# Optimization experiments

Measured on AMD Instinct MI355X. Metric: run time of the kernel, lower is better.

## Reference

```python
import jax, jax.numpy as jnp
import numpy as np

C_CURV = 1.0
EPS = 1e-5            # bound_eps from source
MAX_NORM = (1.0 - 1e-5) / (C_CURV ** 0.5)  # Poincare ball projection radius


def _conv3x3(x, w, b):
    # x: (N,Cin,H,W), w: (Cout,Cin,3,3), padding=1 -> SAME
    y = jax.lax.conv_general_dilated(
        x, w, window_strides=(1, 1), padding=((1, 1), (1, 1)),
        dimension_numbers=('NCHW', 'OIHW', 'NCHW'))
    return y + b[None, :, None, None]


def _maxpool2(x):
    return jax.lax.reduce_window(x, -jnp.inf, jax.lax.max,
                                 (1, 1, 2, 2), (1, 1, 2, 2), 'VALID')


def _hyp_mlr(x, w, b):
    # x: (N,D), w: hyperplane_normals (K,D), b: hyperplane_offsets (K,D)
    c = C_CURV
    sqrt_c = c ** 0.5
    x2 = jnp.sum(x * x, axis=-1, keepdims=True)          # (N,1)
    b2 = jnp.sum(b * b, axis=-1)                          # (K,)
    w_norm = jnp.linalg.norm(w, axis=-1)                  # (K,)
    inner_x_b = x @ (-b.T)                                # (N,K)
    a_num = 1.0 + 2.0 * c * inner_x_b + c * x2            # (N,K)
    b_num = 1.0 - c * b2                                  # (K,)
    denom = 1.0 + 2.0 * c * inner_x_b + (c * c) * (x2 * b2[None, :])
    alpha = a_num / jnp.maximum(denom, EPS)
    beta = b_num[None, :] / denom                         # raw denom, as in source
    mob2 = alpha ** 2 * b2[None, :] + 2.0 * alpha * beta * inner_x_b + beta ** 2 * x2
    sq = jnp.sqrt(mob2)
    normalizer = jnp.where(sq > MAX_NORM, MAX_NORM / jnp.maximum(sq, EPS),
                           jnp.ones_like(mob2))
    mob2 = jnp.where(sq < MAX_NORM, mob2, jnp.full_like(mob2, MAX_NORM ** 2))
    wn = w / jnp.maximum(jnp.linalg.norm(w, axis=-1, keepdims=True), 1e-12)
    hyperplane = alpha * jnp.sum(wn * (-b), axis=-1)[None, :] + beta * (x @ wn.T)
    hyperplane = hyperplane * normalizer
    asinh_in = 2.0 * sqrt_c * hyperplane / jnp.maximum(1.0 - c * mob2, EPS)
    scaler = 2.0 / jnp.maximum(1.0 - c * b2, EPS)         # (K,)
    return (1.0 / sqrt_c) * (scaler * w_norm)[None, :] * jnp.arcsinh(asinh_in)


def setup_inputs() -> dict:
    key = jax.random.key(0)
    ks = jax.random.split(key, 8)
    N, D, K = 4096, 32, 10
    x = jax.random.normal(ks[0], (N, 1, 28, 28), dtype=jnp.float32)
    conv1_w = jax.random.normal(ks[1], (32, 1, 3, 3), dtype=jnp.float32) * 0.1
    conv1_b = jnp.zeros((32,), dtype=jnp.float32)
    conv2_w = jax.random.normal(ks[2], (64, 32, 3, 3), dtype=jnp.float32) * 0.05
    conv2_b = jnp.zeros((64,), dtype=jnp.float32)
    fc_w = jax.random.normal(ks[3], (D, 7 * 7 * 64), dtype=jnp.float32) * 0.02
    fc_b = jnp.zeros((D,), dtype=jnp.float32)
    hyp_w = jax.random.normal(ks[4], (K, D), dtype=jnp.float32) * 0.05
    hyp_b = jnp.zeros((K, D), dtype=jnp.float32)
    return dict(x=x, conv1_w=conv1_w, conv1_b=conv1_b, conv2_w=conv2_w,
                conv2_b=conv2_b, fc_w=fc_w, fc_b=fc_b, hyp_w=hyp_w, hyp_b=hyp_b)


def reference(x, conv1_w, conv1_b, conv2_w, conv2_b, fc_w, fc_b, hyp_w, hyp_b):
    h = _maxpool2(jax.nn.relu(_conv3x3(x, conv1_w, conv1_b)))   # (N,32,14,14)
    h = _maxpool2(jax.nn.relu(_conv3x3(h, conv2_w, conv2_b)))   # (N,64,7,7)
    h = h.reshape(h.shape[0], -1)                                # (N,3136)
    h = h @ fc_w.T + fc_b                                        # (N,32)
    return _hyp_mlr(h, hyp_w, hyp_b)                             # (N,10)
```

## Files before the change

kernel.cpp:

```cpp
#include <hip/hip_runtime.h>
#include <math.h>

#define EPSV 1e-5f

typedef _Float16 f16x8 __attribute__((ext_vector_type(8)));
typedef _Float16 f16x4 __attribute__((ext_vector_type(4)));
typedef float f32x4 __attribute__((ext_vector_type(4)));

__global__ __launch_bounds__(256) void prep_weights(
    const float* __restrict__ w1, const float* __restrict__ b1,
    const float* __restrict__ w2, const float* __restrict__ fw,
    _Float16* __restrict__ w2t_hi, _Float16* __restrict__ w2t_lo,
    _Float16* __restrict__ fw_hi,  _Float16* __restrict__ fw_lo,
    _Float16* __restrict__ w1p_hi, _Float16* __restrict__ w1p_lo)
{
    int idx = blockIdx.x * 256 + threadIdx.x;
    if (idx < 18432) {
        int off = idx >> 11;
        int rem = idx & 2047;
        int oc = rem >> 5, ic = rem & 31;
        float v = w2[(oc * 32 + ic) * 9 + off];
        _Float16 hx = (_Float16)v;
        w2t_hi[idx] = hx;
        w2t_lo[idx] = (_Float16)(v - (float)hx);
    } else if (idx < 18432 + 100352) {
        int j = idx - 18432;
        float v = fw[j];
        _Float16 hx = (_Float16)v;
        fw_hi[j] = hx;
        fw_lo[j] = (_Float16)(v - (float)hx);
    } else if (idx < 18432 + 100352 + 1024) {
        int j = idx - (18432 + 100352);
        int oc = j >> 5, k = j & 31;
        float v = (k < 9) ? w1[oc * 9 + k] : ((k == 9) ? b1[oc] : 0.f);
        _Float16 hx = (_Float16)v;
        w1p_hi[j] = hx;
        w1p_lo[j] = (_Float16)(v - (float)hx);
    }
}

__global__ __launch_bounds__(256, 4) void conv_fused(
    const float* __restrict__ x,
    const _Float16* __restrict__ w1p_hi,
    const _Float16* __restrict__ w1p_lo,
    const _Float16* __restrict__ w2t_hi,
    const _Float16* __restrict__ w2t_lo,
    const float* __restrict__ b2,
    _Float16* __restrict__ feat_hi,
    _Float16* __restrict__ feat_lo)
{
    __shared__ float4 smem4[2017];
    unsigned* in_pad  = (unsigned*)smem4;
    _Float16* Bbuf_hi = (_Float16*)((char*)smem4 + 3600);
    _Float16* Bbuf_lo = (_Float16*)((char*)smem4 + 17936);
    _Float16* Fhi     = (_Float16*)smem4;
    _Float16* Flo     = Fhi + 3136;

    const int tid  = threadIdx.x;
    const int lane = tid & 63;
    const int wave = tid >> 6;
    const int kg   = lane >> 4;
    const int cl   = lane & 15;
    const int clr  = (cl < 14) ? cl : 13;
    const int n    = blockIdx.x;

    for (int i = tid; i < 116; i += 256) {
        int yy, xx;
        if (i < 30)       { yy = 0;          xx = i; }
        else if (i < 60)  { yy = 29;         xx = i - 30; }
        else if (i < 88)  { yy = i - 60 + 1; xx = 0; }
        else              { yy = i - 88 + 1; xx = 29; }
        in_pad[yy * 30 + xx] = 0u;
    }
    const float* xin = x + (size_t)n * 784;
    for (int i = tid; i < 784; i += 256) {
        int yy = i / 28, xx = i - yy * 28;
        float v = xin[i];
        _Float16 hx = (_Float16)v;
        _Float16 lx = (_Float16)(v - (float)hx);
        unsigned hb = *(const unsigned short*)&hx;
        unsigned lb = *(const unsigned short*)&lx;
        in_pad[(yy + 1) * 30 + (xx + 1)] = hb | (lb << 16);
    }
    if (tid < 112) {
        int icg = tid / 28, j = tid - icg * 28;
        int row = j >> 1, col = (j & 1) ? 15 : 0;
        int c = (icg * 224 + row * 16 + col) * 8;
        *(f32x4*)(Bbuf_hi + c) = (f32x4){0.f, 0.f, 0.f, 0.f};
        *(f32x4*)(Bbuf_lo + c) = (f32x4){0.f, 0.f, 0.f, 0.f};
    }
    __syncthreads();

    {
        f16x8 a1h[2], a1l[2];
        #pragma unroll
        for (int m = 0; m < 2; ++m) {
            a1h[m] = *(const f16x8*)(w1p_hi + (m * 16 + cl) * 32 + kg * 8);
            a1l[m] = *(const f16x8*)(w1p_lo + (m * 16 + cl) * 32 + kg * 8);
        }
        const int o0 = (kg == 0) ? 0  : ((kg == 1) ? 62 : 0);
        const int o1 = (kg == 0) ? 1  : 0;
        const int o2 = (kg == 0) ? 2  : 0;
        const int o3 = (kg == 0) ? 30 : 0;
        const int o4 = (kg == 0) ? 31 : 0;
        const int o5 = (kg == 0) ? 32 : 0;
        const int o6 = (kg == 0) ? 60 : 0;
        const int o7 = (kg == 0) ? 61 : 0;

        const bool wr = ((cl & 1) == 0) && (cl < 14);

        #pragma unroll 1
        for (int u = 0; u < 7; ++u) {
            const int unit = wave * 7 + u;
            const int rp = unit >> 1, hx = unit & 1;
            const int xcol = hx * 14 + cl;
            f16x8 bh[2], bl[2];
            #pragma unroll
            for (int r2 = 0; r2 < 2; ++r2) {
                const int base = (2 * rp + r2) * 30 + xcol;
                unsigned v0 = in_pad[base + o0], v1 = in_pad[base + o1];
                unsigned v2 = in_pad[base + o2], v3 = in_pad[base + o3];
                unsigned v4 = in_pad[base + o4], v5 = in_pad[base + o5];
                unsigned v6 = in_pad[base + o6], v7 = in_pad[base + o7];
                unsigned h01 = (v0 & 0xFFFFu) | (v1 << 16);
                unsigned h23 = (v2 & 0xFFFFu) | (v3 << 16);
                unsigned h45 = (v4 & 0xFFFFu) | (v5 << 16);
                unsigned h67 = (v6 & 0xFFFFu) | (v7 << 16);
                unsigned l01 = (v0 >> 16) | (v1 & 0xFFFF0000u);
                unsigned l23 = (v2 >> 16) | (v3 & 0xFFFF0000u);
                unsigned l45 = (v4 >> 16) | (v5 & 0xFFFF0000u);
                unsigned l67 = (v6 >> 16) | (v7 & 0xFFFF0000u);
                if (kg == 1) {
                    h01 = (h01 & 0xFFFFu) | 0x3C000000u;
                    l01 = (l01 & 0xFFFFu);
                    h23 = h45 = h67 = 0u; l23 = l45 = l67 = 0u;
                } else if (kg >= 2) {
                    h01 = h23 = h45 = h67 = 0u;
                    l01 = l23 = l45 = l67 = 0u;
                }
                union { unsigned uu[4]; f16x8 v; } uh, ul;
                uh.uu[0] = h01; uh.uu[1] = h23; uh.uu[2] = h45; uh.uu[3] = h67;
                ul.uu[0] = l01; ul.uu[1] = l23; ul.uu[2] = l45; ul.uu[3] = l67;
                bh[r2] = uh.v; bl[r2] = ul.v;
            }
            #pragma unroll
            for (int m = 0; m < 2; ++m) {
                f32x4 a0 = (f32x4){0.f, 0.f, 0.f, 0.f};
                f32x4 a1 = (f32x4){0.f, 0.f, 0.f, 0.f};
                a0 = __builtin_amdgcn_mfma_f32_16x16x32_f16(a1h[m], bh[0], a0, 0, 0, 0);
                a0 = __builtin_amdgcn_mfma_f32_16x16x32_f16(a1l[m], bh[0], a0, 0, 0, 0);
                a0 = __builtin_amdgcn_mfma_f32_16x16x32_f16(a1h[m], bl[0], a0, 0, 0, 0);
                a1 = __builtin_amdgcn_mfma_f32_16x16x32_f16(a1h[m], bh[1], a1, 0, 0, 0);
                a1 = __builtin_amdgcn_mfma_f32_16x16x32_f16(a1l[m], bh[1], a1, 0, 0, 0);
                a1 = __builtin_amdgcn_mfma_f32_16x16x32_f16(a1h[m], bl[1], a1, 0, 0, 0);
                float pv[4];
                #pragma unroll
                for (int r = 0; r < 4; ++r) {
                    float vp = fmaxf(a0[r], a1[r]);
                    float hp = fmaxf(vp, __shfl_xor(vp, 1));
                    pv[r] = fmaxf(hp, 0.f);
                }
                union { unsigned short s[4]; f16x4 v; } ph, pl;
                #pragma unroll
                for (int r = 0; r < 4; ++r) {
                    _Float16 mh = (_Float16)pv[r];
                    _Float16 ml = (_Float16)(pv[r] - (float)mh);
                    ph.s[r] = *(const unsigned short*)&mh;
                    pl.s[r] = *(const unsigned short*)&ml;
                }
                if (wr) {
                    const int px2 = hx * 7 + (cl >> 1);
                    const int cell = ((m * 2 + (kg >> 1)) * 224 +
                                      rp * 16 + (px2 + 1)) * 8 + (kg & 1) * 4;
                    *(f16x4*)(Bbuf_hi + cell) = ph.v;
                    *(f16x4*)(Bbuf_lo + cell) = pl.v;
                }
            }
        }
    }
    __syncthreads();

    const int ocb = wave * 16;
    float bias[4];
    #pragma unroll
    for (int r = 0; r < 4; ++r) bias[r] = b2[ocb + kg * 4 + r];

    f32x4 acc[14];
    #pragma unroll
    for (int r = 0; r < 14; ++r) acc[r] = (f32x4){0.f, 0.f, 0.f, 0.f};

    {
        const size_t arow = (size_t)(ocb + cl) * 32 + kg * 8;
        f16x8 a_hi = *(const f16x8*)(w2t_hi + arow);
        f16x8 a_lo = *(const f16x8*)(w2t_lo + arow);

        #pragma unroll 1
        for (int off = 0; off < 9; ++off) {
            f16x8 na_hi = a_hi, na_lo = a_lo;
            if (off < 8) {
                na_hi = *(const f16x8*)(w2t_hi + arow + (size_t)(off + 1) * 2048);
                na_lo = *(const f16x8*)(w2t_lo + arow + (size_t)(off + 1) * 2048);
            }
            const int ky = off / 3, kx = off - ky * 3;
            const int cbase = (kg * 224 + clr + kx) * 8;
            #pragma unroll
            for (int py = 0; py < 14; ++py) {
                const int g = ky + py;
                if (g >= 1 && g <= 14) {
                    const int addr = cbase + (g - 1) * 128;
                    f16x8 b_hi = *(const f16x8*)(Bbuf_hi + addr);
                    f16x8 b_lo = *(const f16x8*)(Bbuf_lo + addr);
                    acc[py] = __builtin_amdgcn_mfma_f32_16x16x32_f16(a_hi, b_hi, acc[py], 0, 0, 0);
                    acc[py] = __builtin_amdgcn_mfma_f32_16x16x32_f16(a_lo, b_hi, acc[py], 0, 0, 0);
                    acc[py] = __builtin_amdgcn_mfma_f32_16x16x32_f16(a_hi, b_lo, acc[py], 0, 0, 0);
                }
            }
            a_hi = na_hi; a_lo = na_lo;
        }
    }
    __syncthreads();

    {
        const bool wlane = ((cl & 1) == 0) && (cl < 14);
        const int px2 = cl >> 1;
        #pragma unroll
        for (int p = 0; p < 7; ++p) {
            f32x4 r0 = acc[2 * p], r1 = acc[2 * p + 1];
            #pragma unroll
            for (int r = 0; r < 4; ++r) {
                float v0 = fmaxf(r0[r], __shfl_xor(r0[r], 1));
                float v1 = fmaxf(r1[r], __shfl_xor(r1[r], 1));
                float m = fmaxf(fmaxf(v0, v1) + bias[r], 0.f);
                _Float16 mh = (_Float16)m;
                _Float16 ml = (_Float16)(m - (float)mh);
                if (wlane) {
                    int o = (ocb + kg * 4 + r) * 49 + p * 7 + px2;
                    Fhi[o] = mh; Flo[o] = ml;
                }
            }
        }
    }
    __syncthreads();

    unsigned* gh = (unsigned*)(feat_hi + (size_t)n * 3136);
    unsigned* gl = (unsigned*)(feat_lo + (size_t)n * 3136);
    const unsigned* sh = (const unsigned*)Fhi;
    const unsigned* sl = (const unsigned*)Flo;
    for (int i = tid; i < 1568; i += 256) { gh[i] = sh[i]; gl[i] = sl[i]; }
}

__global__ __launch_bounds__(512) void fc_mlr(
    const _Float16* __restrict__ feat_hi, const _Float16* __restrict__ feat_lo,
    const _Float16* __restrict__ fw_hi,   const _Float16* __restrict__ fw_lo,
    const float* __restrict__ fb,
    const float* __restrict__ hw,
    const float* __restrict__ hb,
    float* __restrict__ out)
{
    __shared__ float part[8][64][9];
    __shared__ float Ht[16][33];

    const int tid  = threadIdx.x;
    const int lane = tid & 63;
    const int wave = tid >> 6;
    const int kg = lane >> 4, cl = lane & 15;
    const int m0 = blockIdx.x * 16;

    const int start = (wave < 2) ? wave * 13 : 26 + (wave - 2) * 12;
    const int nstep = (wave < 2) ? 13 : 12;
    const size_t koff = (size_t)start * 32 + kg * 8;

    const _Float16* ah  = feat_hi + (size_t)(m0 + cl) * 3136 + koff;
    const _Float16* al  = feat_lo + (size_t)(m0 + cl) * 3136 + koff;
    const _Float16* b0h = fw_hi + (size_t)cl * 3136 + koff;
    const _Float16* b0l = fw_lo + (size_t)cl * 3136 + koff;
    const _Float16* b1h = fw_hi + (size_t)(16 + cl) * 3136 + koff;
    const _Float16* b1l = fw_lo + (size_t)(16 + cl) * 3136 + koff;

    f32x4 acc0 = {0.f, 0.f, 0.f, 0.f}, acc1 = {0.f, 0.f, 0.f, 0.f};
    for (int s = 0; s < nstep; ++s) {
        int k0 = s * 32;
        f16x8 vah = *(const f16x8*)(ah + k0);
        f16x8 val_ = *(const f16x8*)(al + k0);
        f16x8 v0h = *(const f16x8*)(b0h + k0);
        f16x8 v0l = *(const f16x8*)(b0l + k0);
        f16x8 v1h = *(const f16x8*)(b1h + k0);
        f16x8 v1l = *(const f16x8*)(b1l + k0);
        acc0 = __builtin_amdgcn_mfma_f32_16x16x32_f16(vah, v0h, acc0, 0, 0, 0);
        acc0 = __builtin_amdgcn_mfma_f32_16x16x32_f16(val_, v0h, acc0, 0, 0, 0);
        acc0 = __builtin_amdgcn_mfma_f32_16x16x32_f16(vah, v0l, acc0, 0, 0, 0);
        acc1 = __builtin_amdgcn_mfma_f32_16x16x32_f16(vah, v1h, acc1, 0, 0, 0);
        acc1 = __builtin_amdgcn_mfma_f32_16x16x32_f16(val_, v1h, acc1, 0, 0, 0);
        acc1 = __builtin_amdgcn_mfma_f32_16x16x32_f16(vah, v1l, acc1, 0, 0, 0);
    }
    #pragma unroll
    for (int r = 0; r < 4; ++r) {
        part[wave][lane][r]     = acc0[r];
        part[wave][lane][4 + r] = acc1[r];
    }
    __syncthreads();

    {
        int col = tid & 31, row = tid >> 5;
        int l  = ((row >> 2) << 4) + (col & 15);
        int rr = ((col >= 16) ? 4 : 0) + (row & 3);
        float s = 0.f;
        #pragma unroll
        for (int w = 0; w < 8; ++w) s += part[w][l][rr];
        Ht[row][col] = s + fb[col];
    }
    __syncthreads();

    if (tid < 160) {
        int im = tid / 10, k = tid - im * 10;
        const float* xr = &Ht[im][0];
        const float* wr = hw + k * 32;
        const float* br = hb + k * 32;
        float x2 = 0.f, b2s = 0.f, ww = 0.f, xb = 0.f, xw = 0.f, wb = 0.f;
        #pragma unroll
        for (int i = 0; i < 32; ++i) {
            float xi = xr[i], wi = wr[i], bi = br[i];
            x2 += xi * xi;  b2s += bi * bi;  ww += wi * wi;
            xb += xi * bi;  xw += xi * wi;   wb += wi * bi;
        }
        float w_norm = sqrtf(ww);
        float wnc = fmaxf(w_norm, 1e-12f);
        float inner = -xb;
        float a_num = 1.f + 2.f * inner + x2;
        float b_num = 1.f - b2s;
        float den = 1.f + 2.f * inner + x2 * b2s;
        float alpha = a_num / fmaxf(den, EPSV);
        float beta = b_num / den;
        float mob2 = alpha * alpha * b2s + 2.f * alpha * beta * inner + beta * beta * x2;
        float sq = sqrtf(mob2);
        const float MAXN = (float)(1.0 - 1e-5);
        const float MAXN2 = (float)((1.0 - 1e-5) * (1.0 - 1e-5));
        float normalizer = (sq > MAXN) ? (MAXN / fmaxf(sq, EPSV)) : 1.f;
        float mob2c = (sq < MAXN) ? mob2 : MAXN2;
        float hyper = (alpha * (-wb) + beta * xw) / wnc;
        hyper *= normalizer;
        float asin_in = 2.f * hyper / fmaxf(1.f - mob2c, EPSV);
        float scaler = 2.f / fmaxf(1.f - b2s, EPSV);
        out[(size_t)m0 * 10 + tid] = scaler * w_norm * asinhf(asin_in);
    }
}

extern "C" void kernel_launch(void* const* d_in, const int* in_sizes, int n_in,
                              void* d_out, int out_size, void* d_ws, size_t ws_size,
                              hipStream_t stream) {
    const float* x   = (const float*)d_in[0];
    const float* w1  = (const float*)d_in[1];
    const float* b1  = (const float*)d_in[2];
    const float* w2  = (const float*)d_in[3];
    const float* b2  = (const float*)d_in[4];
    const float* fw  = (const float*)d_in[5];
    const float* fb  = (const float*)d_in[6];
    const float* hw  = (const float*)d_in[7];
    const float* hb  = (const float*)d_in[8];
    float* out = (float*)d_out;

    const int N = 4096;
    char* ws = (char*)d_ws;
    _Float16* feat_hi = (_Float16*)ws;
    _Float16* feat_lo = (_Float16*)(ws + 25690112);
    _Float16* w2t_hi  = (_Float16*)(ws + 51380224);
    _Float16* w2t_lo  = (_Float16*)(ws + 51417088);
    _Float16* fw_hi   = (_Float16*)(ws + 51453952);
    _Float16* fw_lo   = (_Float16*)(ws + 51654656);
    _Float16* w1p_hi  = (_Float16*)(ws + 51855360);
    _Float16* w1p_lo  = (_Float16*)(ws + 51857408);

    prep_weights<<<(18432 + 100352 + 1024 + 255) / 256, 256, 0, stream>>>(
        w1, b1, w2, fw, w2t_hi, w2t_lo, fw_hi, fw_lo, w1p_hi, w1p_lo);
    conv_fused<<<N, 256, 0, stream>>>(x, w1p_hi, w1p_lo, w2t_hi, w2t_lo, b2,
                                      feat_hi, feat_lo);
    fc_mlr<<<N / 16, 512, 0, stream>>>(feat_hi, feat_lo, fw_hi, fw_lo, fb, hw, hb, out);
}
```

Baseline: 137.7 us.

## Repartition conv2 MFMA work so each wave covers all channels over a row band

Each wave used to own 16 output channels across all 14 output rows. Now it owns all 64 output channels across a band of 4 rows, with the last wave taking 2. Each B fragment loaded from LDS is reused across four A channel-blocks, which cuts LDS reads per MFMA, while A weights are loaded per tap from global memory instead of being prefetched. The work per wave becomes uneven (the last wave has half the rows), and register pressure stays at 16 accumulators.

```diff
diff --git a/kernel.cpp b/kernel.cpp
--- a/kernel.cpp
+++ b/kernel.cpp
@@ -180,42 +180,41 @@
     }
     __syncthreads();
 
-    const int ocb = wave * 16;
-    float bias[4];
+    const int row0 = wave * 4;
+    const int nr   = (wave == 3) ? 2 : 4;
+
+    f32x4 acc[4][4];
     #pragma unroll
-    for (int r = 0; r < 4; ++r) bias[r] = b2[ocb + kg * 4 + r];
-
-    f32x4 acc[14];
-    #pragma unroll
-    for (int r = 0; r < 14; ++r) acc[r] = (f32x4){0.f, 0.f, 0.f, 0.f};
-
-    {
-        const size_t arow = (size_t)(ocb + cl) * 32 + kg * 8;
-        f16x8 a_hi = *(const f16x8*)(w2t_hi + arow);
-        f16x8 a_lo = *(const f16x8*)(w2t_lo + arow);
-
-        #pragma unroll 1
-        for (int off = 0; off < 9; ++off) {
-            f16x8 na_hi = a_hi, na_lo = a_lo;
-            if (off < 8) {
-                na_hi = *(const f16x8*)(w2t_hi + arow + (size_t)(off + 1) * 2048);
-                na_lo = *(const f16x8*)(w2t_lo + arow + (size_t)(off + 1) * 2048);
-            }
-            const int ky = off / 3, kx = off - ky * 3;
-            const int cbase = (kg * 224 + clr + kx) * 8;
-            #pragma unroll
-            for (int py = 0; py < 14; ++py) {
-                const int g = ky + py;
+    for (int m = 0; m < 4; ++m)
+        #pragma unroll
+        for (int pr = 0; pr < 4; ++pr) acc[m][pr] = (f32x4){0.f, 0.f, 0.f, 0.f};
+
+    #pragma unroll 1
+    for (int off = 0; off < 9; ++off) {
+        const int ky = off / 3, kx = off - ky * 3;
+        f16x8 ah[4], al[4];
+        #pragma unroll
+        for (int m = 0; m < 4; ++m) {
+            ah[m] = *(const f16x8*)(w2t_hi + ((size_t)off * 64 + m * 16 + cl) * 32 + kg * 8);
+            al[m] = *(const f16x8*)(w2t_lo + ((size_t)off * 64 + m * 16 + cl) * 32 + kg * 8);
+        }
+        const int cbase = (kg * 224 + clr + kx) * 8;
+        #pragma unroll
+        for (int pr = 0; pr < 4; ++pr) {
+            if (pr < nr) {
+                const int g = row0 + pr + ky;
                 if (g >= 1 && g <= 14) {
                     const int addr = cbase + (g - 1) * 128;
                     f16x8 b_hi = *(const f16x8*)(Bbuf_hi + addr);
                     f16x8 b_lo = *(const f16x8*)(Bbuf_lo + addr);
-                    acc[py] = __builtin_amdgcn_mfma_f32_16x16x32_f16(a_hi, b_hi, acc[py], 0, 0, 0);
-                    acc[py] = __builtin_amdgcn_mfma_f32_16x16x32_f16(a_lo, b_hi, acc[py], 0, 0, 0);
-                    acc[py] = __builtin_amdgcn_mfma_f32_16x16x32_f16(a_hi, b_lo, acc[py], 0, 0, 0);
+                    #pragma unroll
+                    for (int m = 0; m < 4; ++m) {
+                        acc[m][pr] = __builtin_amdgcn_mfma_f32_16x16x32_f16(ah[m], b_hi, acc[m][pr], 0, 0, 0);
+                        acc[m][pr] = __builtin_amdgcn_mfma_f32_16x16x32_f16(al[m], b_hi, acc[m][pr], 0, 0, 0);
+                        acc[m][pr] = __builtin_amdgcn_mfma_f32_16x16x32_f16(ah[m], b_lo, acc[m][pr], 0, 0, 0);
+                    }
                 }
             }
-            a_hi = na_hi; a_lo = na_lo;
         }
     }
     __syncthreads();
@@ -223,19 +222,27 @@
     {
         const bool wlane = ((cl & 1) == 0) && (cl < 14);
         const int px2 = cl >> 1;
-        #pragma unroll
-        for (int p = 0; p < 7; ++p) {
-            f32x4 r0 = acc[2 * p], r1 = acc[2 * p + 1];
+        const int npp = (wave == 3) ? 1 : 2;
+        #pragma unroll
+        for (int m = 0; m < 4; ++m) {
             #pragma unroll
-            for (int r = 0; r < 4; ++r) {
-                float v0 = fmaxf(r0[r], __shfl_xor(r0[r], 1));
-                float v1 = fmaxf(r1[r], __shfl_xor(r1[r], 1));
-                float m = fmaxf(fmaxf(v0, v1) + bias[r], 0.f);
-                _Float16 mh = (_Float16)m;
-                _Float16 ml = (_Float16)(m - (float)mh);
-                if (wlane) {
-                    int o = (ocb + kg * 4 + r) * 49 + p * 7 + px2;
-                    Fhi[o] = mh; Flo[o] = ml;
+            for (int pp = 0; pp < 2; ++pp) {
+                if (pp < npp) {
+                    f32x4 r0 = acc[m][2 * pp], r1 = acc[m][2 * pp + 1];
+                    const int prow = wave * 2 + pp;
+                    #pragma unroll
+                    for (int r = 0; r < 4; ++r) {
+                        const int oc = m * 16 + kg * 4 + r;
+                        float v0 = fmaxf(r0[r], __shfl_xor(r0[r], 1));
+                        float v1 = fmaxf(r1[r], __shfl_xor(r1[r], 1));
+                        float mq = fmaxf(fmaxf(v0, v1) + b2[oc], 0.f);
+                        _Float16 mh = (_Float16)mq;
+                        _Float16 ml = (_Float16)(mq - (float)mh);
+                        if (wlane) {
+                            int o = oc * 49 + prow * 7 + px2;
+                            Fhi[o] = mh; Flo[o] = ml;
+                        }
+                    }
                 }
             }
         }
```

Result: slower. 146.8 us (+6.6%).
